# Kernel optimization log

Measured on AMD Instinct MI355X. Metric: run time of the kernel, lower is better.

## Reference

```python
import jax, jax.numpy as jnp
import numpy as np

OCC_W, SMOOTH_W, SPARSE_W, CONS_W = 1.0, 0.1, 0.01, 0.1
EPS = 1e-7  # torch BCE clamps log terms; clip preds for numerical parity


def setup_inputs() -> dict:
    key = jax.random.key(0)
    k1, k2, k3, k4 = jax.random.split(key, 4)
    N, F = 16384, 64
    predictions = jax.random.uniform(k1, (N,), dtype=jnp.float32, minval=1e-4, maxval=1.0 - 1e-4)
    targets = jax.random.uniform(k2, (N,), dtype=jnp.float32)
    features = jax.random.normal(k3, (N, F), dtype=jnp.float32)
    points = jax.random.normal(k4, (N, 3), dtype=jnp.float32)
    return {"predictions": predictions, "targets": targets, "features": features, "points": points}


def reference(predictions, targets, features, points):
    # --- occupancy loss: BCE(mean) ---
    p = jnp.clip(predictions, EPS, 1.0 - EPS)
    occupancy = -jnp.mean(targets * jnp.log(p) + (1.0 - targets) * jnp.log1p(-p))

    # --- smoothness loss: for each point, 3 nearest neighbors (excl. self) ---
    # Fused all-pairs sq-distance [N, N] + top-k, replacing the per-point python loop.
    sq = jnp.sum(points * points, axis=1)                      # [N]
    d2 = sq[:, None] + sq[None, :] - 2.0 * (points @ points.T)  # [N, N]
    d2 = jnp.maximum(d2, 0.0)  # monotone in distance, so ordering == torch.norm ordering
    _, idx = jax.lax.top_k(-d2, 4)                              # 4 smallest distances
    nn_idx = idx[:, 1:4]                                        # drop self (index 0)
    # per-point local gradient: mean |pred_i - pred_nn|, then mean over points
    smoothness = jnp.mean(jnp.abs(predictions[:, None] - predictions[nn_idx]))

    # --- sparsity loss: mean |features| ---
    sparsity = jnp.mean(jnp.abs(features))

    # --- consistency loss: MSE ---
    consistency = jnp.mean((predictions - targets) ** 2)

    total = (OCC_W * occupancy + SMOOTH_W * smoothness
             + SPARSE_W * sparsity + CONS_W * consistency)
    return total
```

## Files before the change

kernel.cpp:

```cpp
#include <hip/hip_runtime.h>
#include <float.h>
#include <math.h>


constexpr int   N_ = 16384;
constexpr int   F_ = 64;
constexpr float OCC_W = 1.0f, SMOOTH_W = 0.1f, SPARSE_W = 0.01f, CONS_W = 0.1f;
constexpr float EPS_ = 1e-7f;

constexpr int CHUNKS  = 16;
constexpr int CHUNK_J = N_ / CHUNKS;
constexpr int JTILES  = CHUNK_J / 32;
constexpr int IB      = 128;
constexpr int IBLOCKS = N_ / IB;

typedef __attribute__((ext_vector_type(8)))  short bf16x8;
typedef __attribute__((ext_vector_type(16))) float f32x16;

union U128 { uint4 u; bf16x8 s; };

__device__ __forceinline__ void ins4f(float t, float& b0, float& b1, float& b2, float& b3) {
  float n0 = fminf(b0, t);
  float n1 = __builtin_amdgcn_fmed3f(b0, b1, t);
  float n2 = __builtin_amdgcn_fmed3f(b1, b2, t);
  float n3 = __builtin_amdgcn_fmed3f(b2, b3, t);
  b0 = n0; b1 = n1; b2 = n2; b3 = n3;
}

__device__ __forceinline__ void split2(float x, unsigned& h16, unsigned& l16) {
  unsigned u = __float_as_uint(x);
  unsigned r = u + 0x7FFFu + ((u >> 16) & 1u);
  h16 = r >> 16;
  float lo = x - __uint_as_float(r & 0xFFFF0000u);
  unsigned v = __float_as_uint(lo);
  l16 = (v + 0x7FFFu + ((v >> 16) & 1u)) >> 16;
}


__global__ __launch_bounds__(256) void knn_mfma(const float* __restrict__ pts,
                                                float4* __restrict__ cand,
                                                unsigned* __restrict__ done) {
  if (blockIdx.x == 0 && threadIdx.x == 0) *done = 0u;
  __shared__ uint4 AF[2][CHUNK_J];
  const int tid   = threadIdx.x;
  const int chunk = blockIdx.x & (CHUNKS - 1);
  const int ibk   = blockIdx.x >> 4;
  const int j0    = chunk * CHUNK_J;

  for (int t = tid; t < CHUNK_J; t += 256) {
    int j = j0 + t;
    float qx = pts[3 * j], qy = pts[3 * j + 1], qz = pts[3 * j + 2];
    float w  = fmaf(qx, qx, fmaf(qy, qy, qz * qz));
    unsigned Hx, Lx, Hy, Ly, Hz, Lz, Hw, Lw;
    split2(-2.f * qx, Hx, Lx);
    split2(-2.f * qy, Hy, Ly);
    split2(-2.f * qz, Hz, Lz);
    split2(w, Hw, Lw);
    AF[0][t] = make_uint4(Hx | (Hx << 16), Lx | (Lx << 16),
                          Hy | (Hy << 16), Ly | (Ly << 16));
    AF[1][t] = make_uint4(Hz | (Hz << 16), Lz | (Lz << 16),
                          Hw | (Lw << 16), 0u);
  }

  const int lane = tid & 63, wv = tid >> 6;
  const int h = lane >> 5, il = lane & 31;
  const int i = ibk * IB + wv * 32 + il;
  U128 bf;
  {
    float x = pts[3 * i], y = pts[3 * i + 1], z = pts[3 * i + 2];
    unsigned hx, lx, hy, ly, hz, lz;
    split2(x, hx, lx);
    split2(y, hy, ly);
    split2(z, hz, lz);
    if (h == 0) {
      unsigned a = hx | (lx << 16), b = hy | (ly << 16);
      bf.u = make_uint4(a, a, b, b);
    } else {
      unsigned a = hz | (lz << 16);
      bf.u = make_uint4(a, a, 0x3F803F80u, 0u);
    }
  }
  __syncthreads();

  float b0 = FLT_MAX, b1 = FLT_MAX, b2 = FLT_MAX, b3 = FLT_MAX;
  const f32x16 zacc = {};
  const unsigned idb = (unsigned)(chunk * (CHUNK_J / 16));
  const uint4* __restrict__ afp = &AF[h][0];

#pragma unroll 4
  for (int t = 0; t < JTILES; ++t) {
    U128 af; af.u = afp[t * 32 + il];
    f32x16 acc = __builtin_amdgcn_mfma_f32_32x32x16_bf16(af.s, bf.s, zacc, 0, 0, 0);
    float m0 = fminf(fminf(fminf(acc[0], acc[1]), fminf(acc[2], acc[3])),
                     fminf(fminf(acc[4], acc[5]), fminf(acc[6], acc[7])));
    float k0 = __uint_as_float((__float_as_uint(m0) & 0xFFFFFC00u) | (idb + 2u * t));
    ins4f(k0, b0, b1, b2, b3);
    float m1 = fminf(fminf(fminf(acc[8], acc[9]), fminf(acc[10], acc[11])),
                     fminf(fminf(acc[12], acc[13]), fminf(acc[14], acc[15])));
    float k1 = __uint_as_float((__float_as_uint(m1) & 0xFFFFFC00u) | (idb + 2u * t + 1u));
    ins4f(k1, b0, b1, b2, b3);
  }

  float o0 = __shfl_xor(b0, 32), o1 = __shfl_xor(b1, 32),
        o2 = __shfl_xor(b2, 32), o3 = __shfl_xor(b3, 32);
  {
    float B[4] = {b0, b1, b2, b3};
    float O[4] = {o0, o1, o2, o3};
    unsigned ibd[4], iod[4];
#pragma unroll
    for (int k = 0; k < 4; ++k) {
      ibd[k] = __float_as_uint(B[k]) & 0x3FFu;
      iod[k] = __float_as_uint(O[k]) & 0x3FFu;
    }
#pragma unroll
    for (int k = 0; k < 4; ++k) {
#pragma unroll
      for (int m = 0; m < 4; ++m) {
        bool dup = (iod[k] == ibd[m]);
        bool om  = dup && (O[k] >= B[m]);
        bool bm  = dup && (O[k] <  B[m]);
        if (om) O[k] = FLT_MAX;
        if (bm) B[m] = FLT_MAX;
      }
    }
    b0 = b1 = b2 = b3 = FLT_MAX;
#pragma unroll
    for (int k = 0; k < 4; ++k) ins4f(B[k], b0, b1, b2, b3);
#pragma unroll
    for (int k = 0; k < 4; ++k) ins4f(O[k], b0, b1, b2, b3);
  }
  if (h == 0) cand[(size_t)chunk * N_ + i] = make_float4(b0, b1, b2, b3);
}

__global__ __launch_bounds__(256) void merge_kernel(const float* __restrict__ pred,
                                                    const float* __restrict__ targ,
                                                    const float* __restrict__ feat,
                                                    const float* __restrict__ pts,
                                                    const float4* __restrict__ cand,
                                                    float4* __restrict__ part,
                                                    unsigned* __restrict__ done,
                                                    float* __restrict__ out) {
  __shared__ float4 sh[256];
  __shared__ float ws4[4][4];
  __shared__ int is_last;
  constexpr int CPT = CHUNKS / 4;
  int tid  = threadIdx.x;
  int lane = tid & 63;
  int sub  = tid >> 6;
  int i = blockIdx.x * 64 + lane;

  const float4* f4 = (const float4*)feat;
  float s_sp = 0.f;
#pragma unroll
  for (int s = 0; s < 4; ++s) {
    float4 v = f4[(size_t)s * 65536 + blockIdx.x * 256 + tid];
    s_sp += fabsf(v.x) + fabsf(v.y) + fabsf(v.z) + fabsf(v.w);
  }

  float b0 = FLT_MAX, b1 = FLT_MAX, b2 = FLT_MAX, b3 = FLT_MAX;
#pragma unroll
  for (int cc = 0; cc < CPT; ++cc) {
    float4 v = cand[(size_t)(sub * CPT + cc) * N_ + i];
    ins4f(v.x, b0, b1, b2, b3);
    ins4f(v.y, b0, b1, b2, b3);
    ins4f(v.z, b0, b1, b2, b3);
    ins4f(v.w, b0, b1, b2, b3);
  }
  sh[tid] = make_float4(b0, b1, b2, b3);
  __syncthreads();

  float s_occ = 0.f, s_cons = 0.f, s_sm = 0.f;
  if (sub == 0) {
#pragma unroll
    for (int w = 1; w < 4; ++w) {
      float4 v = sh[w * 64 + lane];
      ins4f(v.x, b0, b1, b2, b3);
      ins4f(v.y, b0, b1, b2, b3);
      ins4f(v.z, b0, b1, b2, b3);
      ins4f(v.w, b0, b1, b2, b3);
    }
    unsigned qarr[4] = {__float_as_uint(b0) & 0x3FFu, __float_as_uint(b1) & 0x3FFu,
                        __float_as_uint(b2) & 0x3FFu, __float_as_uint(b3) & 0x3FFu};
    float xi = pts[3 * i], yi = pts[3 * i + 1], zi = pts[3 * i + 2];
    float c0 = FLT_MAX, c1 = FLT_MAX, c2 = FLT_MAX;
    float p0 = 0.f, p1 = 0.f, p2 = 0.f;
#pragma unroll
    for (int s = 0; s < 4; ++s) {
#pragma unroll 8
      for (int m = 0; m < 16; ++m) {
        int j = (int)(qarr[s] * 16 + m);
        float dx = xi - pts[3 * j], dy = yi - pts[3 * j + 1], dz = zi - pts[3 * j + 2];
        float d2 = fmaf(dx, dx, fmaf(dy, dy, dz * dz));
        float pj = pred[j];
        if (j != i && d2 < c2) {
          bool cc0 = d2 < c0, cc1 = d2 < c1;
          float n2 = cc1 ? c1 : d2;               float m2 = cc1 ? p1 : pj;
          float n1 = cc0 ? c0 : (cc1 ? d2 : c1);  float m1 = cc0 ? p0 : (cc1 ? pj : p1);
          float n0 = cc0 ? d2 : c0;               float m0 = cc0 ? pj : p0;
          c0 = n0; c1 = n1; c2 = n2; p0 = m0; p1 = m1; p2 = m2;
        }
      }
    }
    float pi = pred[i], tg = targ[i];
    float p  = fminf(fmaxf(pi, EPS_), 1.0f - EPS_);
    s_occ  = -(tg * __logf(p) + (1.0f - tg) * __logf(1.0f - p));
    float dd = pi - tg;
    s_cons = dd * dd;
    s_sm   = fabsf(pi - p0) + fabsf(pi - p1) + fabsf(pi - p2);
  }

  for (int off = 32; off > 0; off >>= 1) {
    s_sp   += __shfl_down(s_sp, off);
    s_occ  += __shfl_down(s_occ, off);
    s_cons += __shfl_down(s_cons, off);
    s_sm   += __shfl_down(s_sm, off);
  }
  if ((tid & 63) == 0) {
    int w = tid >> 6;
    ws4[w][0] = s_occ; ws4[w][1] = s_cons; ws4[w][2] = s_sp; ws4[w][3] = s_sm;
  }
  __syncthreads();
  if (tid == 0) {
    part[blockIdx.x] = make_float4(ws4[0][0] + ws4[1][0] + ws4[2][0] + ws4[3][0],
                                   ws4[0][1] + ws4[1][1] + ws4[2][1] + ws4[3][1],
                                   ws4[0][2] + ws4[1][2] + ws4[2][2] + ws4[3][2],
                                   ws4[0][3] + ws4[1][3] + ws4[2][3] + ws4[3][3]);
    __threadfence();
    unsigned prev = atomicAdd(done, 1u);
    is_last = (prev == (unsigned)(gridDim.x - 1));
  }
  __syncthreads();

  if (is_last) {
    __threadfence();
    float4 a = part[tid];
    float o = a.x, cn = a.y, sp = a.z, sm = a.w;
    for (int off = 32; off > 0; off >>= 1) {
      o  += __shfl_down(o, off);
      cn += __shfl_down(cn, off);
      sp += __shfl_down(sp, off);
      sm += __shfl_down(sm, off);
    }
    if ((tid & 63) == 0) {
      int w = tid >> 6;
      ws4[w][0] = o; ws4[w][1] = cn; ws4[w][2] = sp; ws4[w][3] = sm;
    }
    __syncthreads();
    if (tid == 0) {
      float occ  = ws4[0][0] + ws4[1][0] + ws4[2][0] + ws4[3][0];
      float cons = ws4[0][1] + ws4[1][1] + ws4[2][1] + ws4[3][1];
      float spar = ws4[0][2] + ws4[1][2] + ws4[2][2] + ws4[3][2];
      float smoo = ws4[0][3] + ws4[1][3] + ws4[2][3] + ws4[3][3];
      out[0] = OCC_W * (occ / (float)N_)
             + CONS_W * (cons / (float)N_)
             + SPARSE_W * (spar / (float)(N_ * F_))
             + SMOOTH_W * (smoo / (float)(N_ * 3));
    }
  }
}

extern "C" void kernel_launch(void* const* d_in, const int* in_sizes, int n_in,
                              void* d_out, int out_size, void* d_ws, size_t ws_size,
                              hipStream_t stream) {
  const float* pred = (const float*)d_in[0];
  const float* targ = (const float*)d_in[1];
  const float* feat = (const float*)d_in[2];
  const float* pts  = (const float*)d_in[3];
  float* out = (float*)d_out;

  char*     ws   = (char*)d_ws;
  float4*   part = (float4*)ws;
  unsigned* done = (unsigned*)(ws + 4096);
  float4*   cand = (float4*)(ws + 8192);

  knn_mfma<<<IBLOCKS * CHUNKS, 256, 0, stream>>>(pts, cand, done);
  merge_kernel<<<256, 256, 0, stream>>>(pred, targ, feat, pts, cand, part, done, out);
}
```

Before: 112.0 us.

## Split exact-distance refinement across four waves and reorder tile min reductions

In the merge kernel, every wave now computes the full top-4 candidate tiles, and each wave exactly rescans one of the four 16-point tiles. Per-wave top-3 results are exchanged through shared memory and merged by wave 0. Previously wave 0 alone scanned all 64 candidates, so this spreads the serial gather and compare work over four times as many lanes. In the main kernel the min-reduction over MFMA outputs becomes a linear chain and both tile keys are computed before insertion. The cost is an extra barrier, added shared memory, and redundant candidate merging in every wave.

Result: faster. 100.5 us (-10.3%).

```diff
diff --git a/kernel.cpp b/kernel.cpp
--- a/kernel.cpp
+++ b/kernel.cpp
@@ -91,13 +91,13 @@
   for (int t = 0; t < JTILES; ++t) {
     U128 af; af.u = afp[t * 32 + il];
     f32x16 acc = __builtin_amdgcn_mfma_f32_32x32x16_bf16(af.s, bf.s, zacc, 0, 0, 0);
-    float m0 = fminf(fminf(fminf(acc[0], acc[1]), fminf(acc[2], acc[3])),
-                     fminf(fminf(acc[4], acc[5]), fminf(acc[6], acc[7])));
+    float m0 = fminf(fminf(fminf(fminf(fminf(fminf(fminf(
+                  acc[0], acc[1]), acc[2]), acc[3]), acc[4]), acc[5]), acc[6]), acc[7]);
+    float m1 = fminf(fminf(fminf(fminf(fminf(fminf(fminf(
+                  acc[8], acc[9]), acc[10]), acc[11]), acc[12]), acc[13]), acc[14]), acc[15]);
     float k0 = __uint_as_float((__float_as_uint(m0) & 0xFFFFFC00u) | (idb + 2u * t));
+    float k1 = __uint_as_float((__float_as_uint(m1) & 0xFFFFFC00u) | (idb + 2u * t + 1u));
     ins4f(k0, b0, b1, b2, b3);
-    float m1 = fminf(fminf(fminf(acc[8], acc[9]), fminf(acc[10], acc[11])),
-                     fminf(fminf(acc[12], acc[13]), fminf(acc[14], acc[15])));
-    float k1 = __uint_as_float((__float_as_uint(m1) & 0xFFFFFC00u) | (idb + 2u * t + 1u));
     ins4f(k1, b0, b1, b2, b3);
   }
 
@@ -141,6 +141,7 @@
                                                     unsigned* __restrict__ done,
                                                     float* __restrict__ out) {
   __shared__ float4 sh[256];
+  __shared__ float2 t3[4][3][64];
   __shared__ float ws4[4][4];
   __shared__ int is_last;
   constexpr int CPT = CHUNKS / 4;
@@ -169,30 +170,52 @@
   sh[tid] = make_float4(b0, b1, b2, b3);
   __syncthreads();
 
+  b0 = b1 = b2 = b3 = FLT_MAX;
+#pragma unroll
+  for (int w = 0; w < 4; ++w) {
+    float4 v = sh[w * 64 + lane];
+    ins4f(v.x, b0, b1, b2, b3);
+    ins4f(v.y, b0, b1, b2, b3);
+    ins4f(v.z, b0, b1, b2, b3);
+    ins4f(v.w, b0, b1, b2, b3);
+  }
+  unsigned qsel;
+  {
+    float bsel = sub == 0 ? b0 : (sub == 1 ? b1 : (sub == 2 ? b2 : b3));
+    qsel = __float_as_uint(bsel) & 0x3FFu;
+  }
+
+  float xi = pts[3 * i], yi = pts[3 * i + 1], zi = pts[3 * i + 2];
+  float c0 = FLT_MAX, c1 = FLT_MAX, c2 = FLT_MAX;
+  float p0 = 0.f, p1 = 0.f, p2 = 0.f;
+#pragma unroll 8
+  for (int m = 0; m < 16; ++m) {
+    int j = (int)(qsel * 16 + m);
+    float dx = xi - pts[3 * j], dy = yi - pts[3 * j + 1], dz = zi - pts[3 * j + 2];
+    float d2 = fmaf(dx, dx, fmaf(dy, dy, dz * dz));
+    float pj = pred[j];
+    if (j != i && d2 < c2) {
+      bool cc0 = d2 < c0, cc1 = d2 < c1;
+      float n2 = cc1 ? c1 : d2;               float m2 = cc1 ? p1 : pj;
+      float n1 = cc0 ? c0 : (cc1 ? d2 : c1);  float m1 = cc0 ? p0 : (cc1 ? pj : p1);
+      float n0 = cc0 ? d2 : c0;               float m0 = cc0 ? pj : p0;
+      c0 = n0; c1 = n1; c2 = n2; p0 = m0; p1 = m1; p2 = m2;
+    }
+  }
+  t3[sub][0][lane] = make_float2(c0, p0);
+  t3[sub][1][lane] = make_float2(c1, p1);
+  t3[sub][2][lane] = make_float2(c2, p2);
+  __syncthreads();
+
   float s_occ = 0.f, s_cons = 0.f, s_sm = 0.f;
   if (sub == 0) {
 #pragma unroll
     for (int w = 1; w < 4; ++w) {
-      float4 v = sh[w * 64 + lane];
-      ins4f(v.x, b0, b1, b2, b3);
-      ins4f(v.y, b0, b1, b2, b3);
-      ins4f(v.z, b0, b1, b2, b3);
-      ins4f(v.w, b0, b1, b2, b3);
-    }
-    unsigned qarr[4] = {__float_as_uint(b0) & 0x3FFu, __float_as_uint(b1) & 0x3FFu,
-                        __float_as_uint(b2) & 0x3FFu, __float_as_uint(b3) & 0x3FFu};
-    float xi = pts[3 * i], yi = pts[3 * i + 1], zi = pts[3 * i + 2];
-    float c0 = FLT_MAX, c1 = FLT_MAX, c2 = FLT_MAX;
-    float p0 = 0.f, p1 = 0.f, p2 = 0.f;
-#pragma unroll
-    for (int s = 0; s < 4; ++s) {
-#pragma unroll 8
-      for (int m = 0; m < 16; ++m) {
-        int j = (int)(qarr[s] * 16 + m);
-        float dx = xi - pts[3 * j], dy = yi - pts[3 * j + 1], dz = zi - pts[3 * j + 2];
-        float d2 = fmaf(dx, dx, fmaf(dy, dy, dz * dz));
-        float pj = pred[j];
-        if (j != i && d2 < c2) {
+#pragma unroll
+      for (int r = 0; r < 3; ++r) {
+        float2 e = t3[w][r][lane];
+        float d2 = e.x, pj = e.y;
+        if (d2 < c2) {
           bool cc0 = d2 < c0, cc1 = d2 < c1;
           float n2 = cc1 ? c1 : d2;               float m2 = cc1 ? p1 : pj;
           float n1 = cc0 ? c0 : (cc1 ? d2 : c1);  float m1 = cc0 ? p0 : (cc1 ? pj : p1);
```

## Fuse kNN candidate search and merge into one kernel with per-row-block tickets

Applied to the files above, without the earlier changes.

Merges the MFMA kNN candidate kernel and the merge/reduction kernel into a single launch. The last chunk block to finish for each row block, chosen with an atomic ticket, does that block's candidate merge, exact refinement and loss terms. The sparsity sum is spread across all blocks. Candidate granularity coarsens from 16-column to 32-column groups with one key per tile, which halves the ins4f inserts in the hot loop but doubles the exact refinement scan, now split across two half-blocks. It adds a memset launch and atomic/fence overhead, and only 128 blocks do the tail work.

Result: slower. 340.9 us (+204.3%).

```diff
diff --git a/kernel.cpp b/kernel.cpp
--- a/kernel.cpp
+++ b/kernel.cpp
@@ -25,6 +25,18 @@
   float n2 = __builtin_amdgcn_fmed3f(b1, b2, t);
   float n3 = __builtin_amdgcn_fmed3f(b2, b3, t);
   b0 = n0; b1 = n1; b2 = n2; b3 = n3;
+}
+
+__device__ __forceinline__ void ins3dp(float d2, float pj,
+                                       float& c0, float& c1, float& c2,
+                                       float& p0, float& p1, float& p2) {
+  if (d2 < c2) {
+    bool cc0 = d2 < c0, cc1 = d2 < c1;
+    float n2 = cc1 ? c1 : d2;               float m2 = cc1 ? p1 : pj;
+    float n1 = cc0 ? c0 : (cc1 ? d2 : c1);  float m1 = cc0 ? p0 : (cc1 ? pj : p1);
+    float n0 = cc0 ? d2 : c0;               float m0 = cc0 ? pj : p0;
+    c0 = n0; c1 = n1; c2 = n2; p0 = m0; p1 = m1; p2 = m2;
+  }
 }
 
 __device__ __forceinline__ void split2(float x, unsigned& h16, unsigned& l16) {
@@ -37,16 +49,36 @@
 }
 
 
-__global__ __launch_bounds__(256) void knn_mfma(const float* __restrict__ pts,
-                                                float4* __restrict__ cand,
-                                                unsigned* __restrict__ done) {
-  if (blockIdx.x == 0 && threadIdx.x == 0) *done = 0u;
-  __shared__ uint4 AF[2][CHUNK_J];
+__global__ __launch_bounds__(256) void fused_kernel(const float* __restrict__ pred,
+                                                    const float* __restrict__ targ,
+                                                    const float* __restrict__ feat,
+                                                    const float* __restrict__ pts,
+                                                    float4* __restrict__ part,
+                                                    unsigned* __restrict__ done,
+                                                    unsigned* __restrict__ ticket,
+                                                    float* __restrict__ featp,
+                                                    float4* __restrict__ cand,
+                                                    float* __restrict__ out) {
+  __shared__ __align__(16) unsigned char smem[32768];
+  __shared__ float fws[4];
+  __shared__ float ws4[4][4];
+  __shared__ int mflag, lflag;
+
   const int tid   = threadIdx.x;
-  const int chunk = blockIdx.x & (CHUNKS - 1);
-  const int ibk   = blockIdx.x >> 4;
+  const int b     = blockIdx.x;
+  const int chunk = b & (CHUNKS - 1);
+  const int ibk   = b >> 4;
   const int j0    = chunk * CHUNK_J;
-
+  const int lane  = tid & 63, wv = tid >> 6;
+  const int h     = lane >> 5, il = lane & 31;
+
+  {
+    float a = fabsf(feat[b * 512 + tid]) + fabsf(feat[b * 512 + 256 + tid]);
+    for (int off = 32; off > 0; off >>= 1) a += __shfl_down(a, off);
+    if (lane == 0) fws[wv] = a;
+  }
+
+  uint4 (*AF)[CHUNK_J] = reinterpret_cast<uint4(*)[CHUNK_J]>(smem);
   for (int t = tid; t < CHUNK_J; t += 256) {
     int j = j0 + t;
     float qx = pts[3 * j], qy = pts[3 * j + 1], qz = pts[3 * j + 2];
@@ -62,10 +94,8 @@
                           Hw | (Lw << 16), 0u);
   }
 
-  const int lane = tid & 63, wv = tid >> 6;
-  const int h = lane >> 5, il = lane & 31;
   const int i = ibk * IB + wv * 32 + il;
-  U128 bf;
+  U128 bfr;
   {
     float x = pts[3 * i], y = pts[3 * i + 1], z = pts[3 * i + 2];
     unsigned hx, lx, hy, ly, hz, lz;
@@ -73,44 +103,46 @@
     split2(y, hy, ly);
     split2(z, hz, lz);
     if (h == 0) {
-      unsigned a = hx | (lx << 16), b = hy | (ly << 16);
-      bf.u = make_uint4(a, a, b, b);
+      unsigned a = hx | (lx << 16), c = hy | (ly << 16);
+      bfr.u = make_uint4(a, a, c, c);
     } else {
       unsigned a = hz | (lz << 16);
-      bf.u = make_uint4(a, a, 0x3F803F80u, 0u);
-    }
-  }
-  __syncthreads();
+      bfr.u = make_uint4(a, a, 0x3F803F80u, 0u);
+    }
+  }
+  __syncthreads();
+  if (tid == 0) featp[b] = fws[0] + fws[1] + fws[2] + fws[3];
 
   float b0 = FLT_MAX, b1 = FLT_MAX, b2 = FLT_MAX, b3 = FLT_MAX;
   const f32x16 zacc = {};
-  const unsigned idb = (unsigned)(chunk * (CHUNK_J / 16));
+  const unsigned idb = (unsigned)(chunk * JTILES);
   const uint4* __restrict__ afp = &AF[h][0];
 
 #pragma unroll 4
   for (int t = 0; t < JTILES; ++t) {
     U128 af; af.u = afp[t * 32 + il];
-    f32x16 acc = __builtin_amdgcn_mfma_f32_32x32x16_bf16(af.s, bf.s, zacc, 0, 0, 0);
-    float m0 = fminf(fminf(fminf(acc[0], acc[1]), fminf(acc[2], acc[3])),
-                     fminf(fminf(acc[4], acc[5]), fminf(acc[6], acc[7])));
-    float k0 = __uint_as_float((__float_as_uint(m0) & 0xFFFFFC00u) | (idb + 2u * t));
-    ins4f(k0, b0, b1, b2, b3);
-    float m1 = fminf(fminf(fminf(acc[8], acc[9]), fminf(acc[10], acc[11])),
-                     fminf(fminf(acc[12], acc[13]), fminf(acc[14], acc[15])));
-    float k1 = __uint_as_float((__float_as_uint(m1) & 0xFFFFFC00u) | (idb + 2u * t + 1u));
-    ins4f(k1, b0, b1, b2, b3);
-  }
-
-  float o0 = __shfl_xor(b0, 32), o1 = __shfl_xor(b1, 32),
-        o2 = __shfl_xor(b2, 32), o3 = __shfl_xor(b3, 32);
+    f32x16 acc = __builtin_amdgcn_mfma_f32_32x32x16_bf16(af.s, bfr.s, zacc, 0, 0, 0);
+    float u0 = fminf(acc[0],  acc[1]),  u1 = fminf(acc[2],  acc[3]);
+    float u2 = fminf(acc[4],  acc[5]),  u3 = fminf(acc[6],  acc[7]);
+    float u4 = fminf(acc[8],  acc[9]),  u5 = fminf(acc[10], acc[11]);
+    float u6 = fminf(acc[12], acc[13]), u7 = fminf(acc[14], acc[15]);
+    float v0 = fminf(u0, u1), v1 = fminf(u2, u3);
+    float v2 = fminf(u4, u5), v3 = fminf(u6, u7);
+    float m  = fminf(fminf(v0, v1), fminf(v2, v3));
+    float kf = __uint_as_float((__float_as_uint(m) & 0xFFFFFE00u) | (idb + (unsigned)t));
+    ins4f(kf, b0, b1, b2, b3);
+  }
+
   {
+    float o0 = __shfl_xor(b0, 32), o1 = __shfl_xor(b1, 32),
+          o2 = __shfl_xor(b2, 32), o3 = __shfl_xor(b3, 32);
     float B[4] = {b0, b1, b2, b3};
     float O[4] = {o0, o1, o2, o3};
     unsigned ibd[4], iod[4];
 #pragma unroll
     for (int k = 0; k < 4; ++k) {
-      ibd[k] = __float_as_uint(B[k]) & 0x3FFu;
-      iod[k] = __float_as_uint(O[k]) & 0x3FFu;
+      ibd[k] = __float_as_uint(B[k]) & 0x1FFu;
+      iod[k] = __float_as_uint(O[k]) & 0x1FFu;
     }
 #pragma unroll
     for (int k = 0; k < 4; ++k) {
@@ -130,132 +162,129 @@
     for (int k = 0; k < 4; ++k) ins4f(O[k], b0, b1, b2, b3);
   }
   if (h == 0) cand[(size_t)chunk * N_ + i] = make_float4(b0, b1, b2, b3);
-}
-
-__global__ __launch_bounds__(256) void merge_kernel(const float* __restrict__ pred,
-                                                    const float* __restrict__ targ,
-                                                    const float* __restrict__ feat,
-                                                    const float* __restrict__ pts,
-                                                    const float4* __restrict__ cand,
-                                                    float4* __restrict__ part,
-                                                    unsigned* __restrict__ done,
-                                                    float* __restrict__ out) {
-  __shared__ float4 sh[256];
-  __shared__ float ws4[4][4];
-  __shared__ int is_last;
-  constexpr int CPT = CHUNKS / 4;
-  int tid  = threadIdx.x;
-  int lane = tid & 63;
-  int sub  = tid >> 6;
-  int i = blockIdx.x * 64 + lane;
-
-  const float4* f4 = (const float4*)feat;
-  float s_sp = 0.f;
-#pragma unroll
-  for (int s = 0; s < 4; ++s) {
-    float4 v = f4[(size_t)s * 65536 + blockIdx.x * 256 + tid];
-    s_sp += fabsf(v.x) + fabsf(v.y) + fabsf(v.z) + fabsf(v.w);
-  }
-
-  float b0 = FLT_MAX, b1 = FLT_MAX, b2 = FLT_MAX, b3 = FLT_MAX;
-#pragma unroll
-  for (int cc = 0; cc < CPT; ++cc) {
-    float4 v = cand[(size_t)(sub * CPT + cc) * N_ + i];
-    ins4f(v.x, b0, b1, b2, b3);
-    ins4f(v.y, b0, b1, b2, b3);
-    ins4f(v.z, b0, b1, b2, b3);
-    ins4f(v.w, b0, b1, b2, b3);
-  }
-  sh[tid] = make_float4(b0, b1, b2, b3);
+
+  __threadfence();
+  __syncthreads();
+  if (tid == 0) {
+    unsigned prev = atomicAdd(&ticket[ibk], 1u);
+    mflag = (prev == (unsigned)(CHUNKS - 1));
+  }
+  __syncthreads();
+  if (!mflag) return;
+  __threadfence();
+
+  float4* pb = reinterpret_cast<float4*>(smem);
+  uint4*  tg = reinterpret_cast<uint4*>(smem + 4096);
+  float2* t3 = reinterpret_cast<float2*>(smem + 8192);
+
+  const int ii   = tid & 127, half = tid >> 7;
+  const int iG   = ibk * IB + ii;
+
+  float a0 = FLT_MAX, a1 = FLT_MAX, a2 = FLT_MAX, a3 = FLT_MAX;
+#pragma unroll
+  for (int cc = 0; cc < 8; ++cc) {
+    float4 v = cand[(size_t)(half * 8 + cc) * N_ + iG];
+    ins4f(v.x, a0, a1, a2, a3);
+    ins4f(v.y, a0, a1, a2, a3);
+    ins4f(v.z, a0, a1, a2, a3);
+    ins4f(v.w, a0, a1, a2, a3);
+  }
+  pb[half * 128 + ii] = make_float4(a0, a1, a2, a3);
+  __syncthreads();
+
+  if (half == 0) {
+    float4 o = pb[128 + ii];
+    ins4f(o.x, a0, a1, a2, a3);
+    ins4f(o.y, a0, a1, a2, a3);
+    ins4f(o.z, a0, a1, a2, a3);
+    ins4f(o.w, a0, a1, a2, a3);
+    tg[ii] = make_uint4(__float_as_uint(a0) & 0x1FFu, __float_as_uint(a1) & 0x1FFu,
+                        __float_as_uint(a2) & 0x1FFu, __float_as_uint(a3) & 0x1FFu);
+  }
+  __syncthreads();
+
+  uint4 g4 = tg[ii];
+  unsigned ga = half ? g4.z : g4.x;
+  unsigned gb = half ? g4.w : g4.y;
+  float xi = pts[3 * iG], yi = pts[3 * iG + 1], zi = pts[3 * iG + 2];
+  float c0 = FLT_MAX, c1 = FLT_MAX, c2 = FLT_MAX;
+  float p0 = 0.f, p1 = 0.f, p2 = 0.f;
+#pragma unroll 1
+  for (int gsel = 0; gsel < 2; ++gsel) {
+    int jb = (int)(gsel ? gb : ga) * 32;
+#pragma unroll 8
+    for (int m = 0; m < 32; ++m) {
+      int j = jb + m;
+      float dx = xi - pts[3 * j], dy = yi - pts[3 * j + 1], dz = zi - pts[3 * j + 2];
+      float d2 = fmaf(dx, dx, fmaf(dy, dy, dz * dz));
+      float pj = pred[j];
+      if (j != iG) ins3dp(d2, pj, c0, c1, c2, p0, p1, p2);
+    }
+  }
+  t3[(half * 3 + 0) * 128 + ii] = make_float2(c0, p0);
+  t3[(half * 3 + 1) * 128 + ii] = make_float2(c1, p1);
+  t3[(half * 3 + 2) * 128 + ii] = make_float2(c2, p2);
   __syncthreads();
 
   float s_occ = 0.f, s_cons = 0.f, s_sm = 0.f;
-  if (sub == 0) {
-#pragma unroll
-    for (int w = 1; w < 4; ++w) {
-      float4 v = sh[w * 64 + lane];
-      ins4f(v.x, b0, b1, b2, b3);
-      ins4f(v.y, b0, b1, b2, b3);
-      ins4f(v.z, b0, b1, b2, b3);
-      ins4f(v.w, b0, b1, b2, b3);
-    }
-    unsigned qarr[4] = {__float_as_uint(b0) & 0x3FFu, __float_as_uint(b1) & 0x3FFu,
-                        __float_as_uint(b2) & 0x3FFu, __float_as_uint(b3) & 0x3FFu};
-    float xi = pts[3 * i], yi = pts[3 * i + 1], zi = pts[3 * i + 2];
-    float c0 = FLT_MAX, c1 = FLT_MAX, c2 = FLT_MAX;
-    float p0 = 0.f, p1 = 0.f, p2 = 0.f;
-#pragma unroll
-    for (int s = 0; s < 4; ++s) {
-#pragma unroll 8
-      for (int m = 0; m < 16; ++m) {
-        int j = (int)(qarr[s] * 16 + m);
-        float dx = xi - pts[3 * j], dy = yi - pts[3 * j + 1], dz = zi - pts[3 * j + 2];
-        float d2 = fmaf(dx, dx, fmaf(dy, dy, dz * dz));
-        float pj = pred[j];
-        if (j != i && d2 < c2) {
-          bool cc0 = d2 < c0, cc1 = d2 < c1;
-          float n2 = cc1 ? c1 : d2;               float m2 = cc1 ? p1 : pj;
-          float n1 = cc0 ? c0 : (cc1 ? d2 : c1);  float m1 = cc0 ? p0 : (cc1 ? pj : p1);
-          float n0 = cc0 ? d2 : c0;               float m0 = cc0 ? pj : p0;
-          c0 = n0; c1 = n1; c2 = n2; p0 = m0; p1 = m1; p2 = m2;
-        }
-      }
-    }
-    float pi = pred[i], tg = targ[i];
+  if (half == 0) {
+#pragma unroll
+    for (int r = 0; r < 3; ++r) {
+      float2 e = t3[(3 + r) * 128 + ii];
+      ins3dp(e.x, e.y, c0, c1, c2, p0, p1, p2);
+    }
+    float pi = pred[iG], tgv = targ[iG];
     float p  = fminf(fmaxf(pi, EPS_), 1.0f - EPS_);
-    s_occ  = -(tg * __logf(p) + (1.0f - tg) * __logf(1.0f - p));
-    float dd = pi - tg;
+    s_occ  = -(tgv * __logf(p) + (1.0f - tgv) * __logf(1.0f - p));
+    float dd = pi - tgv;
     s_cons = dd * dd;
     s_sm   = fabsf(pi - p0) + fabsf(pi - p1) + fabsf(pi - p2);
   }
 
   for (int off = 32; off > 0; off >>= 1) {
-    s_sp   += __shfl_down(s_sp, off);
     s_occ  += __shfl_down(s_occ, off);
     s_cons += __shfl_down(s_cons, off);
     s_sm   += __shfl_down(s_sm, off);
   }
-  if ((tid & 63) == 0) {
-    int w = tid >> 6;
-    ws4[w][0] = s_occ; ws4[w][1] = s_cons; ws4[w][2] = s_sp; ws4[w][3] = s_sm;
-  }
+  if (lane == 0) { ws4[wv][0] = s_occ; ws4[wv][1] = s_cons; ws4[wv][2] = s_sm; }
   __syncthreads();
   if (tid == 0) {
-    part[blockIdx.x] = make_float4(ws4[0][0] + ws4[1][0] + ws4[2][0] + ws4[3][0],
-                                   ws4[0][1] + ws4[1][1] + ws4[2][1] + ws4[3][1],
-                                   ws4[0][2] + ws4[1][2] + ws4[2][2] + ws4[3][2],
-                                   ws4[0][3] + ws4[1][3] + ws4[2][3] + ws4[3][3]);
+    part[ibk] = make_float4(ws4[0][0] + ws4[1][0] + ws4[2][0] + ws4[3][0],
+                            ws4[0][1] + ws4[1][1] + ws4[2][1] + ws4[3][1],
+                            0.f,
+                            ws4[0][2] + ws4[1][2] + ws4[2][2] + ws4[3][2]);
     __threadfence();
     unsigned prev = atomicAdd(done, 1u);
-    is_last = (prev == (unsigned)(gridDim.x - 1));
-  }
-  __syncthreads();
-
-  if (is_last) {
-    __threadfence();
+    lflag = (prev == (unsigned)(IBLOCKS - 1));
+  }
+  __syncthreads();
+  if (!lflag) return;
+  __threadfence();
+
+  float fo = 0.f, fc = 0.f, fs = 0.f, fp = 0.f;
+  if (tid < IBLOCKS) {
     float4 a = part[tid];
-    float o = a.x, cn = a.y, sp = a.z, sm = a.w;
-    for (int off = 32; off > 0; off >>= 1) {
-      o  += __shfl_down(o, off);
-      cn += __shfl_down(cn, off);
-      sp += __shfl_down(sp, off);
-      sm += __shfl_down(sm, off);
-    }
-    if ((tid & 63) == 0) {
-      int w = tid >> 6;
-      ws4[w][0] = o; ws4[w][1] = cn; ws4[w][2] = sp; ws4[w][3] = sm;
-    }
-    __syncthreads();
-    if (tid == 0) {
-      float occ  = ws4[0][0] + ws4[1][0] + ws4[2][0] + ws4[3][0];
-      float cons = ws4[0][1] + ws4[1][1] + ws4[2][1] + ws4[3][1];
-      float spar = ws4[0][2] + ws4[1][2] + ws4[2][2] + ws4[3][2];
-      float smoo = ws4[0][3] + ws4[1][3] + ws4[2][3] + ws4[3][3];
-      out[0] = OCC_W * (occ / (float)N_)
-             + CONS_W * (cons / (float)N_)
-             + SPARSE_W * (spar / (float)(N_ * F_))
-             + SMOOTH_W * (smoo / (float)(N_ * 3));
-    }
+    fo = a.x; fc = a.y; fs = a.w;
+  }
+#pragma unroll
+  for (int q = 0; q < 8; ++q) fp += featp[tid * 8 + q];
+  for (int off = 32; off > 0; off >>= 1) {
+    fo += __shfl_down(fo, off);
+    fc += __shfl_down(fc, off);
+    fs += __shfl_down(fs, off);
+    fp += __shfl_down(fp, off);
+  }
+  if (lane == 0) { ws4[wv][0] = fo; ws4[wv][1] = fc; ws4[wv][2] = fs; ws4[wv][3] = fp; }
+  __syncthreads();
+  if (tid == 0) {
+    float occ  = ws4[0][0] + ws4[1][0] + ws4[2][0] + ws4[3][0];
+    float cons = ws4[0][1] + ws4[1][1] + ws4[2][1] + ws4[3][1];
+    float smoo = ws4[0][2] + ws4[1][2] + ws4[2][2] + ws4[3][2];
+    float spar = ws4[0][3] + ws4[1][3] + ws4[2][3] + ws4[3][3];
+    out[0] = OCC_W * (occ / (float)N_)
+           + CONS_W * (cons / (float)N_)
+           + SPARSE_W * (spar / (float)(N_ * F_))
+           + SMOOTH_W * (smoo / (float)(N_ * 3));
   }
 }
 
@@ -268,11 +297,15 @@
   const float* pts  = (const float*)d_in[3];
   float* out = (float*)d_out;
 
-  char*     ws   = (char*)d_ws;
-  float4*   part = (float4*)ws;
-  unsigned* done = (unsigned*)(ws + 4096);
-  float4*   cand = (float4*)(ws + 8192);
-
-  knn_mfma<<<IBLOCKS * CHUNKS, 256, 0, stream>>>(pts, cand, done);
-  merge_kernel<<<256, 256, 0, stream>>>(pred, targ, feat, pts, cand, part, done, out);
-}
+  char*     ws     = (char*)d_ws;
+  float4*   part   = (float4*)ws;
+  unsigned* done   = (unsigned*)(ws + 4096);
+  unsigned* ticket = (unsigned*)(ws + 4100);
+  float*    featp  = (float*)(ws + 5120);
+  float4*   cand   = (float4*)(ws + 16384);
+
+  hipMemsetAsync(ws + 4096, 0, 4 + 4 * IBLOCKS, stream);
+  fused_kernel<<<IBLOCKS * CHUNKS, 256, 0, stream>>>(pred, targ, feat, pts,
+                                                     part, done, ticket, featp,
+                                                     cand, out);
+}
```
